# Kernel tuning notes

Hardware: AMD Instinct MI355X
Metric: run time of the kernel (lower is better)

Reference implementation:

```python
import jax, jax.numpy as jnp
import numpy as np

B, S, E, H = 16, 1024, 256, 8
DH = E // H


def layer_norm(x, g, b, eps=1e-5):
    m = jnp.mean(x, axis=-1, keepdims=True)
    v = jnp.mean(jnp.square(x - m), axis=-1, keepdims=True)
    return (x - m) * jax.lax.rsqrt(v + eps) * g + b


def setup_inputs() -> dict:
    key = jax.random.key(0)
    ks = jax.random.split(key, 8)
    w = 1.0 / np.sqrt(E)
    return {
        "Matrix": jax.random.normal(ks[0], (B, S, E), jnp.float32),
        "ln_g": jnp.ones((E,), jnp.float32),
        "ln_b": jnp.zeros((E,), jnp.float32),
        "Wq": jax.random.normal(ks[1], (E, E), jnp.float32) * w,
        "bq": jnp.zeros((E,), jnp.float32),
        "Wk": jax.random.normal(ks[2], (E, E), jnp.float32) * w,
        "bk": jnp.zeros((E,), jnp.float32),
        "Wv": jax.random.normal(ks[3], (E, E), jnp.float32) * w,
        "bv": jnp.zeros((E,), jnp.float32),
        "Wo": jax.random.normal(ks[4], (E, E), jnp.float32) * w,
        "bo": jnp.zeros((E,), jnp.float32),
        "rel_bias": jax.random.normal(ks[5], (S, S), jnp.float32) * 0.02,
        "gW": jax.random.normal(ks[6], (E, E), jnp.float32) * w,
        "gb": jnp.zeros((E,), jnp.float32),
        "mW": jax.random.normal(ks[7], (E, E), jnp.float32) * w,
        "mb": jnp.zeros((E,), jnp.float32),
    }


def relation_mha(x, Wq, bq, Wk, bk, Wv, bv, Wo, bo, rel_bias):
    # x: [B,S,E]; self-attention q=k=v=x with additive per-game-pair bias
    def heads(t):
        return t.reshape(B, S, H, DH).transpose(0, 2, 1, 3)  # [B,H,S,DH]
    q = heads(x @ Wq + bq)
    k = heads(x @ Wk + bk)
    v = heads(x @ Wv + bv)
    scores = jnp.einsum("bhqd,bhkd->bhqk", q, k) / np.sqrt(DH)
    scores = scores + rel_bias[None, None, :, :]  # relational bias over game pairs
    attn = jax.nn.softmax(scores, axis=-1)
    o = jnp.einsum("bhqk,bhkd->bhqd", attn, v)
    o = o.transpose(0, 2, 1, 3).reshape(B, S, E)
    return o @ Wo + bo


def reference(Matrix, ln_g, ln_b, Wq, bq, Wk, bk, Wv, bv, Wo, bo, rel_bias, gW, gb, mW, mb):
    ln = layer_norm(Matrix, ln_g, ln_b)
    rmha = relation_mha(ln, Wq, bq, Wk, bk, Wv, bv, Wo, bo, rel_bias)
    gate0 = jax.nn.sigmoid(Matrix @ gW + gb)
    gate1 = gate0 * rmha + Matrix
    mlp = jax.nn.sigmoid(gate1 @ mW + mb)
    final = gate1 * layer_norm(mlp, ln_g, ln_b) + gate1
    return final
```

## Files before the change

### kernel.cpp

```cpp
#include <hip/hip_runtime.h>
#include <hip/hip_bf16.h>


#define BB 16
#define SS 1024
#define EE 256
#define HH 8
#define DHD 32
#define MM (BB*SS)

typedef __attribute__((ext_vector_type(8))) short bf16x8;
typedef __attribute__((ext_vector_type(4))) float f32x4;
typedef __attribute__((ext_vector_type(4))) unsigned short u16x4;
typedef __attribute__((ext_vector_type(4))) _Float16 h16x4;
typedef __attribute__((ext_vector_type(8))) _Float16 h16x8;
typedef __attribute__((ext_vector_type(2))) _Float16 h16x2;

__device__ __forceinline__ float bf2f(unsigned short u){
  unsigned int x = ((unsigned int)u) << 16;
  return __builtin_bit_cast(float, x);
}
__device__ __forceinline__ unsigned short f2bf(float f){
  unsigned int x = __builtin_bit_cast(unsigned int, f);
  return (unsigned short)((x + 0x7FFFu + ((x >> 16) & 1u)) >> 16);
}

struct SP { const void* s[8]; };
__global__ __launch_bounds__(256) void conv_small(SP sp, unsigned short* __restrict__ dst,
    const unsigned int* __restrict__ lraw){
  bool isbf = (lraw[0] != 0x3F800000u);
  int a = blockIdx.x, t = threadIdx.x;
  const void* s = sp.s[a];
  dst[a*256 + t] = isbf ? ((const unsigned short*)s)[t] : f2bf(((const float*)s)[t]);
}

struct WSP { const void* s[6]; };
__global__ __launch_bounds__(256) void transp_w(WSP wp, unsigned short* __restrict__ dst,
    const unsigned int* __restrict__ lraw){
  __shared__ float T[64][65];
  bool isbf = (lraw[0] != 0x3F800000u);
  int w = blockIdx.z, k0 = blockIdx.x*64, n0 = blockIdx.y*64;
  int tx = threadIdx.x & 63, ty = threadIdx.x >> 6;
  const void* s = wp.s[w];
  #pragma unroll
  for (int r = ty; r < 64; r += 4)
    T[r][tx] = isbf ? bf2f(((const unsigned short*)s)[(k0+r)*EE + n0+tx])
                    : ((const float*)s)[(k0+r)*EE + n0+tx];
  __syncthreads();
  #pragma unroll
  for (int r = ty; r < 64; r += 4)
    dst[(size_t)w*EE*EE + (size_t)(n0+r)*EE + k0+tx] = f2bf(T[tx][r]);
}

__global__ __launch_bounds__(256) void rbh_prep(const void* __restrict__ src,
    unsigned short* __restrict__ dst, const unsigned int* __restrict__ lraw){
  bool isbf = (lraw[0] != 0x3F800000u);
  int idx = blockIdx.x*256 + threadIdx.x;
  int k4 = idx & (SS/4 - 1), q = idx >> 8;
  int k = k4*4;
  const float LOG2E = 1.4426950408889634f;
  float4 v;
  if (isbf){
    u16x4 u = ((const u16x4*)src)[idx];
    v.x = bf2f(u.x); v.y = bf2f(u.y); v.z = bf2f(u.z); v.w = bf2f(u.w);
  } else {
    v = ((const float4*)src)[idx];
  }
  u16x4 o;
  o.x = f2bf(v.x*LOG2E); o.y = f2bf(v.y*LOG2E);
  o.z = f2bf(v.z*LOG2E); o.w = f2bf(v.w*LOG2E);
  size_t base = ((size_t)(k >> 4)*SS + q)*16 + (k & 15);
  *(u16x4*)&dst[base] = o;
}

__global__ __launch_bounds__(256) void ln_x(const void* __restrict__ Mraw,
    const unsigned short* __restrict__ g, const unsigned short* __restrict__ b,
    unsigned short* __restrict__ Xc, unsigned short* __restrict__ LNout,
    const unsigned int* __restrict__ lraw){
  int wave = threadIdx.x >> 6, lane = threadIdx.x & 63;
  size_t row = (size_t)blockIdx.x*4 + wave;
  int col = lane*4;
  bool isbf = (lraw[0] != 0x3F800000u);
  float x0, x1, x2, x3;
  if (isbf){
    u16x4 xu = *(const u16x4*)((const unsigned short*)Mraw + row*EE + col);
    x0 = bf2f(xu.x); x1 = bf2f(xu.y); x2 = bf2f(xu.z); x3 = bf2f(xu.w);
  } else {
    float4 xv = *(const float4*)((const float*)Mraw + row*EE + col);
    x0 = xv.x; x1 = xv.y; x2 = xv.z; x3 = xv.w;
  }
  u16x4 xo; xo.x = f2bf(x0); xo.y = f2bf(x1); xo.z = f2bf(x2); xo.w = f2bf(x3);
  *(u16x4*)(Xc + row*EE + col) = xo;
  float s = (x0+x1)+(x2+x3);
  float s2 = (x0*x0+x1*x1)+(x2*x2+x3*x3);
  #pragma unroll
  for (int o = 32; o >= 1; o >>= 1){ s += __shfl_xor(s, o, 64); s2 += __shfl_xor(s2, o, 64); }
  float m = s*(1.0f/EE);
  float var = s2*(1.0f/EE) - m*m;
  float rstd = rsqrtf(var + 1e-5f);
  u16x4 gu = *(const u16x4*)(g + col), bu = *(const u16x4*)(b + col);
  u16x4 o;
  o.x = f2bf((x0-m)*rstd*bf2f(gu.x) + bf2f(bu.x));
  o.y = f2bf((x1-m)*rstd*bf2f(gu.y) + bf2f(bu.y));
  o.z = f2bf((x2-m)*rstd*bf2f(gu.z) + bf2f(bu.z));
  o.w = f2bf((x3-m)*rstd*bf2f(gu.w) + bf2f(bu.w));
  *(u16x4*)(LNout + row*EE + col) = o;
}

__global__ __launch_bounds__(256, 2) void qkv_gemm(const unsigned short* __restrict__ LN,
    const unsigned short* __restrict__ WqT, const unsigned short* __restrict__ WkT,
    const unsigned short* __restrict__ WvT, const unsigned short* __restrict__ bq,
    const unsigned short* __restrict__ bk, const unsigned short* __restrict__ bv,
    _Float16* __restrict__ Qh, _Float16* __restrict__ Kh, _Float16* __restrict__ Vf){
  int tid = threadIdx.x, wave = tid >> 6, lane = tid & 63, quad = lane >> 4, l16 = lane & 15;
  int mw = blockIdx.x*256 + wave*64;
  int n0 = blockIdx.y*32;
  const float QSCL = 0.2550348663f;
  f32x4 aq[4][2] = {}, ak[4][2] = {}, av[4][2] = {};
  const unsigned short* Ap = LN + (size_t)mw*EE;
  #pragma unroll
  for (int k0 = 0; k0 < EE; k0 += 32){
    bf16x8 a[4], b1[2], b2[2], b3[2];
    #pragma unroll
    for (int mf = 0; mf < 4; mf++)
      a[mf] = *(const bf16x8*)(Ap + (size_t)(mf*16 + l16)*EE + k0 + quad*8);
    #pragma unroll
    for (int nt = 0; nt < 2; nt++){
      b1[nt] = *(const bf16x8*)(WqT + (size_t)(n0 + nt*16 + l16)*EE + k0 + quad*8);
      b2[nt] = *(const bf16x8*)(WkT + (size_t)(n0 + nt*16 + l16)*EE + k0 + quad*8);
      b3[nt] = *(const bf16x8*)(WvT + (size_t)(n0 + nt*16 + l16)*EE + k0 + quad*8);
    }
    #pragma unroll
    for (int mf = 0; mf < 4; mf++)
      #pragma unroll
      for (int nt = 0; nt < 2; nt++){
        aq[mf][nt] = __builtin_amdgcn_mfma_f32_16x16x32_bf16(a[mf], b1[nt], aq[mf][nt], 0, 0, 0);
        ak[mf][nt] = __builtin_amdgcn_mfma_f32_16x16x32_bf16(a[mf], b2[nt], ak[mf][nt], 0, 0, 0);
        av[mf][nt] = __builtin_amdgcn_mfma_f32_16x16x32_bf16(a[mf], b3[nt], av[mf][nt], 0, 0, 0);
      }
  }
  int sblk = mw & 1023, bb = mw >> 10;
  #pragma unroll
  for (int nt = 0; nt < 2; nt++){
    int col = n0 + nt*16 + l16, hh = col >> 5, dd = col & 31;
    float bqv = bf2f(bq[col]), bkv = bf2f(bk[col]), bvv = bf2f(bv[col]);
    size_t bhh = (size_t)(bb*HH + hh);
    #pragma unroll
    for (int mf = 0; mf < 4; mf++){
      int s0 = sblk + mf*16 + quad*4;
      h16x4 vv;
      #pragma unroll
      for (int r = 0; r < 4; r++) vv[r] = (_Float16)(av[mf][nt][r] + bvv);
      *(h16x4*)(Vf + ((bhh*64 + (s0 >> 4))*DHD + dd)*16 + (s0 & 15)) = vv;
      #pragma unroll
      for (int r = 0; r < 4; r++){
        size_t o = (bhh*SS + s0 + r)*DHD + dd;
        Qh[o] = (_Float16)((aq[mf][nt][r] + bqv) * QSCL);
        Kh[o] = (_Float16)(ak[mf][nt][r] + bkv);
      }
    }
  }
}

__global__ __launch_bounds__(256) void attn(const _Float16* __restrict__ Qh,
    const _Float16* __restrict__ Kh, const _Float16* __restrict__ Vf,
    const unsigned short* __restrict__ RBh, unsigned short* __restrict__ O){
  int qt = blockIdx.x, h = blockIdx.y, b = blockIdx.z;
  int tid = threadIdx.x, wave = tid >> 6, lane = tid & 63, quad = lane >> 4, l16 = lane & 15;
  int q0 = qt*128 + wave*32;
  const size_t bh = (size_t)(b*HH + h);

  h16x8 qb[2];
  qb[0] = *(const h16x8*)(Qh + (bh*SS + q0 +      l16)*DHD + quad*8);
  qb[1] = *(const h16x8*)(Qh + (bh*SS + q0 + 16 + l16)*DHD + quad*8);

  const _Float16* kp = Kh + (bh*SS + l16)*DHD + quad*8;
  const _Float16* vp = Vf + (bh*64*DHD + l16)*16 + quad*4;
  const unsigned short* rp0 = RBh + ((size_t)0*SS + q0 + l16)*16 + quad*4;
  const unsigned short* rp1 = RBh + ((size_t)1*SS + q0 + l16)*16 + quad*4;
  const unsigned short* rp2 = RBh + ((size_t)2*SS + q0 + l16)*16 + quad*4;
  const unsigned short* rp3 = RBh + ((size_t)3*SS + q0 + l16)*16 + quad*4;

  f32x4 oacc[2][2] = {};
  f32x4 lac[2] = {};

  h16x8 kf[4];
  u16x4 rbu[4][2];
  kf[0] = *(const h16x8*)(kp +    0);
  kf[1] = *(const h16x8*)(kp +  512);
  kf[2] = *(const h16x8*)(kp + 1024);
  kf[3] = *(const h16x8*)(kp + 1536);
  rbu[0][0] = *(const u16x4*)(rp0); rbu[0][1] = *(const u16x4*)(rp0 + 256);
  rbu[1][0] = *(const u16x4*)(rp1); rbu[1][1] = *(const u16x4*)(rp1 + 256);
  rbu[2][0] = *(const u16x4*)(rp2); rbu[2][1] = *(const u16x4*)(rp2 + 256);
  rbu[3][0] = *(const u16x4*)(rp3); rbu[3][1] = *(const u16x4*)(rp3 + 256);
  kp += 2048; rp0 += 65536; rp1 += 65536; rp2 += 65536; rp3 += 65536;

  for (int kt = 0; kt < 16; kt++){
    h16x4 vf[4][2];
    #pragma unroll
    for (int c = 0; c < 4; c++){
      vf[c][0] = *(const h16x4*)(vp + (c*2    )*256);
      vf[c][1] = *(const h16x4*)(vp + (c*2 + 1)*256);
    }
    h16x8 kn[4];
    u16x4 rbn[4][2];
    if (kt < 15){
      kn[0] = *(const h16x8*)(kp +    0);
      kn[1] = *(const h16x8*)(kp +  512);
      kn[2] = *(const h16x8*)(kp + 1024);
      kn[3] = *(const h16x8*)(kp + 1536);
      rbn[0][0] = *(const u16x4*)(rp0); rbn[0][1] = *(const u16x4*)(rp0 + 256);
      rbn[1][0] = *(const u16x4*)(rp1); rbn[1][1] = *(const u16x4*)(rp1 + 256);
      rbn[2][0] = *(const u16x4*)(rp2); rbn[2][1] = *(const u16x4*)(rp2 + 256);
      rbn[3][0] = *(const u16x4*)(rp3); rbn[3][1] = *(const u16x4*)(rp3 + 256);
    }
    #pragma unroll
    for (int c = 0; c < 4; c++){
      #pragma unroll
      for (int qf = 0; qf < 2; qf++){
        f32x4 rb;
        rb[0] = bf2f(rbu[c][qf].x); rb[1] = bf2f(rbu[c][qf].y);
        rb[2] = bf2f(rbu[c][qf].z); rb[3] = bf2f(rbu[c][qf].w);
        f32x4 st = __builtin_amdgcn_mfma_f32_16x16x32_f16(kf[c], qb[qf], rb, 0, 0, 0);
        f32x4 p;
        p[0] = __builtin_amdgcn_exp2f(st[0]);
        p[1] = __builtin_amdgcn_exp2f(st[1]);
        p[2] = __builtin_amdgcn_exp2f(st[2]);
        p[3] = __builtin_amdgcn_exp2f(st[3]);
        lac[qf] += p;
        h16x2 lo = __builtin_bit_cast(h16x2, __builtin_amdgcn_cvt_pkrtz(p[0], p[1]));
        h16x2 hi = __builtin_bit_cast(h16x2, __builtin_amdgcn_cvt_pkrtz(p[2], p[3]));
        h16x4 pf; pf[0] = lo[0]; pf[1] = lo[1]; pf[2] = hi[0]; pf[3] = hi[1];
        oacc[qf][0] = __builtin_amdgcn_mfma_f32_16x16x16f16(pf, vf[c][0], oacc[qf][0], 0, 0, 0);
        oacc[qf][1] = __builtin_amdgcn_mfma_f32_16x16x16f16(pf, vf[c][1], oacc[qf][1], 0, 0, 0);
      }
    }
    #pragma unroll
    for (int c = 0; c < 4; c++){
      kf[c] = kn[c];
      rbu[c][0] = rbn[c][0]; rbu[c][1] = rbn[c][1];
    }
    kp += 2048; vp += 2048;
    rp0 += 65536; rp1 += 65536; rp2 += 65536; rp3 += 65536;
  }
  float lsum[2];
  #pragma unroll
  for (int qf = 0; qf < 2; qf++){
    float l = (lac[qf][0] + lac[qf][1]) + (lac[qf][2] + lac[qf][3]);
    l += __shfl_xor(l, 16, 64);
    l += __shfl_xor(l, 32, 64);
    lsum[qf] = l;
  }
  #pragma unroll
  for (int qf = 0; qf < 2; qf++)
    #pragma unroll
    for (int r = 0; r < 4; r++){
      float linv = 1.0f / __shfl(lsum[qf], quad*4 + r, 64);
      int q = q0 + qf*16 + quad*4 + r;
      #pragma unroll
      for (int dt = 0; dt < 2; dt++)
        O[((size_t)(b*SS + q))*EE + h*DHD + dt*16 + l16] = f2bf(oacc[qf][dt][r] * linv);
    }
}

__global__ __launch_bounds__(256, 2) void og_gemm(const unsigned short* __restrict__ AO,
    const unsigned short* __restrict__ Xc, const unsigned short* __restrict__ WoT,
    const unsigned short* __restrict__ gWT, const unsigned short* __restrict__ bo,
    const unsigned short* __restrict__ gb, unsigned short* __restrict__ G1b){
  int tid = threadIdx.x, wave = tid >> 6, lane = tid & 63, quad = lane >> 4, l16 = lane & 15;
  int mw = blockIdx.x*256 + wave*64;
  int n0 = blockIdx.y*32;
  f32x4 ro[4][2] = {}, rg[4][2] = {};
  #pragma unroll
  for (int k0 = 0; k0 < EE; k0 += 32){
    bf16x8 a1[4], a2[4], b1[2], b2[2];
    #pragma unroll
    for (int mf = 0; mf < 4; mf++){
      a1[mf] = *(const bf16x8*)(AO + (size_t)(mw + mf*16 + l16)*EE + k0 + quad*8);
      a2[mf] = *(const bf16x8*)(Xc + (size_t)(mw + mf*16 + l16)*EE + k0 + quad*8);
    }
    #pragma unroll
    for (int nt = 0; nt < 2; nt++){
      b1[nt] = *(const bf16x8*)(WoT + (size_t)(n0 + nt*16 + l16)*EE + k0 + quad*8);
      b2[nt] = *(const bf16x8*)(gWT + (size_t)(n0 + nt*16 + l16)*EE + k0 + quad*8);
    }
    #pragma unroll
    for (int mf = 0; mf < 4; mf++)
      #pragma unroll
      for (int nt = 0; nt < 2; nt++){
        ro[mf][nt] = __builtin_amdgcn_mfma_f32_16x16x32_bf16(a1[mf], b1[nt], ro[mf][nt], 0, 0, 0);
        rg[mf][nt] = __builtin_amdgcn_mfma_f32_16x16x32_bf16(a2[mf], b2[nt], rg[mf][nt], 0, 0, 0);
      }
  }
  #pragma unroll
  for (int nt = 0; nt < 2; nt++){
    int col = n0 + nt*16 + l16;
    float bov = bf2f(bo[col]), gbv = bf2f(gb[col]);
    #pragma unroll
    for (int mf = 0; mf < 4; mf++)
      #pragma unroll
      for (int r = 0; r < 4; r++){
        size_t row = (size_t)(mw + mf*16 + quad*4 + r);
        float rm  = ro[mf][nt][r] + bov;
        float g0p = rg[mf][nt][r] + gbv;
        float g0  = 1.0f / (1.0f + __expf(-g0p));
        float x   = bf2f(Xc[row*EE + col]);
        G1b[row*EE + col] = f2bf(g0*rm + x);
      }
  }
}

__global__ __launch_bounds__(256, 4) void mlp_final(const unsigned short* __restrict__ G1,
    const unsigned short* __restrict__ Wt, const unsigned short* __restrict__ bias,
    const unsigned short* __restrict__ g, const unsigned short* __restrict__ b,
    void* __restrict__ out, const unsigned int* __restrict__ lraw){
  __shared__ float red[4][16][2];
  int tid = threadIdx.x, wave = tid >> 6, lane = tid & 63, quad = lane >> 4, l16 = lane & 15;
  int m0 = blockIdx.x*16;
  int n0 = wave*64;
  f32x4 acc[4] = {};
  const unsigned short* Ap = G1 + (size_t)(m0 + l16)*EE + quad*8;
  #pragma unroll
  for (int k0 = 0; k0 < EE; k0 += 32){
    bf16x8 a = *(const bf16x8*)(Ap + k0);
    #pragma unroll
    for (int nt = 0; nt < 4; nt++){
      bf16x8 bb = *(const bf16x8*)(Wt + (size_t)(n0 + nt*16 + l16)*EE + k0 + quad*8);
      acc[nt] = __builtin_amdgcn_mfma_f32_16x16x32_bf16(a, bb, acc[nt], 0, 0, 0);
    }
  }
  #pragma unroll
  for (int nt = 0; nt < 4; nt++){
    float bv = bf2f(bias[n0 + nt*16 + l16]);
    #pragma unroll
    for (int r = 0; r < 4; r++)
      acc[nt][r] = 1.0f / (1.0f + __expf(-(acc[nt][r] + bv)));
  }
  #pragma unroll
  for (int r = 0; r < 4; r++){
    float s  = (acc[0][r] + acc[1][r]) + (acc[2][r] + acc[3][r]);
    float sq = (acc[0][r]*acc[0][r] + acc[1][r]*acc[1][r])
             + (acc[2][r]*acc[2][r] + acc[3][r]*acc[3][r]);
    #pragma unroll
    for (int o = 8; o >= 1; o >>= 1){ s += __shfl_xor(s, o, 64); sq += __shfl_xor(sq, o, 64); }
    if (l16 == 0){ red[wave][quad*4 + r][0] = s; red[wave][quad*4 + r][1] = sq; }
  }
  __syncthreads();
  bool isbf = (lraw[0] != 0x3F800000u);
  #pragma unroll
  for (int r = 0; r < 4; r++){
    int rowl = quad*4 + r;
    float s  = (red[0][rowl][0] + red[1][rowl][0]) + (red[2][rowl][0] + red[3][rowl][0]);
    float sq = (red[0][rowl][1] + red[1][rowl][1]) + (red[2][rowl][1] + red[3][rowl][1]);
    float m = s*(1.0f/EE);
    float var = sq*(1.0f/EE) - m*m;
    float rstd = rsqrtf(var + 1e-5f);
    size_t row = (size_t)(m0 + rowl);
    #pragma unroll
    for (int nt = 0; nt < 4; nt++){
      int col = n0 + nt*16 + l16;
      float ln = (acc[nt][r] - m)*rstd*bf2f(g[col]) + bf2f(b[col]);
      float g1 = bf2f(G1[row*EE + col]);
      float y = g1*ln + g1;
      if (isbf) ((unsigned short*)out)[row*EE + col] = f2bf(y);
      else      ((float*)out)[row*EE + col] = y;
    }
  }
}

extern "C" void kernel_launch(void* const* d_in, const int* in_sizes, int n_in,
                              void* d_out, int out_size, void* d_ws, size_t ws_size,
                              hipStream_t stream) {
  (void)in_sizes; (void)n_in; (void)out_size; (void)ws_size;
  const unsigned int* lraw = (const unsigned int*)d_in[1];

  char* ws = (char*)d_ws;
  size_t off = 0;
  auto alloc = [&](size_t bytes)->char*{
    char* p = ws + off; off += (bytes + 255) & ~(size_t)255; return p;
  };
  unsigned short* Xc  = (unsigned short*)alloc((size_t)MM*EE*2);
  unsigned short* RBh = (unsigned short*)alloc((size_t)SS*SS*2);
  unsigned short* SM  = (unsigned short*)alloc(8*256*2);
  unsigned short* Wt  = (unsigned short*)alloc((size_t)6*EE*EE*2);
  unsigned short* LNb = (unsigned short*)alloc((size_t)MM*EE*2);
  _Float16*       Qh  = (_Float16*)alloc((size_t)MM*EE*2);
  _Float16*       Kh  = (_Float16*)alloc((size_t)MM*EE*2);
  _Float16*       Vf  = (_Float16*)alloc((size_t)MM*EE*2);
  unsigned short* AOut= (unsigned short*)alloc((size_t)MM*EE*2);
  unsigned short* G1b = (unsigned short*)alloc((size_t)MM*EE*2);

  dim3 b256(256);
  SP sp = {{ d_in[1], d_in[2], d_in[4], d_in[6], d_in[8], d_in[10], d_in[13], d_in[15] }};
  conv_small<<<dim3(8), b256, 0, stream>>>(sp, SM, lraw);
  WSP wp = {{ d_in[3], d_in[5], d_in[7], d_in[9], d_in[12], d_in[14] }};
  transp_w<<<dim3(4, 4, 6), b256, 0, stream>>>(wp, Wt, lraw);
  rbh_prep<<<dim3(SS*SS/4/256), b256, 0, stream>>>(d_in[11], RBh, lraw);

  ln_x<<<dim3(MM/4), b256, 0, stream>>>(d_in[0], SM + 0*256, SM + 1*256, Xc, LNb, lraw);

  qkv_gemm<<<dim3(64, 8), b256, 0, stream>>>(LNb, Wt + 0*EE*EE, Wt + 1*EE*EE, Wt + 2*EE*EE,
                                             SM + 2*256, SM + 3*256, SM + 4*256, Qh, Kh, Vf);

  attn<<<dim3(8, 8, 16), b256, 0, stream>>>(Qh, Kh, Vf, RBh, AOut);

  og_gemm<<<dim3(64, 8), b256, 0, stream>>>(AOut, Xc, Wt + 3*EE*EE, Wt + 4*EE*EE,
                                            SM + 5*256, SM + 6*256, G1b);

  mlp_final<<<dim3(MM/16), b256, 0, stream>>>(G1b, Wt + 5*EE*EE, SM + 7*256,
                                              SM + 0*256, SM + 1*256, d_out, lraw);
}
```

Measured before the change: 238.3 us.

## Shrink attention per-wave query tile to 16 rows and reorder grid by head

```diff
diff --git a/kernel.cpp b/kernel.cpp
--- a/kernel.cpp
+++ b/kernel.cpp
@@ -162,106 +162,83 @@
   }
 }
 
-__global__ __launch_bounds__(256) void attn(const _Float16* __restrict__ Qh,
+__global__ __launch_bounds__(256, 6) void attn(const _Float16* __restrict__ Qh,
     const _Float16* __restrict__ Kh, const _Float16* __restrict__ Vf,
     const unsigned short* __restrict__ RBh, unsigned short* __restrict__ O){
-  int qt = blockIdx.x, h = blockIdx.y, b = blockIdx.z;
+  int h = blockIdx.x, qt = blockIdx.y, b = blockIdx.z;
   int tid = threadIdx.x, wave = tid >> 6, lane = tid & 63, quad = lane >> 4, l16 = lane & 15;
-  int q0 = qt*128 + wave*32;
+  int q0 = qt*64 + wave*16;
   const size_t bh = (size_t)(b*HH + h);
 
-  h16x8 qb[2];
-  qb[0] = *(const h16x8*)(Qh + (bh*SS + q0 +      l16)*DHD + quad*8);
-  qb[1] = *(const h16x8*)(Qh + (bh*SS + q0 + 16 + l16)*DHD + quad*8);
+  h16x8 qb = *(const h16x8*)(Qh + (bh*SS + q0 + l16)*DHD + quad*8);
 
   const _Float16* kp = Kh + (bh*SS + l16)*DHD + quad*8;
   const _Float16* vp = Vf + (bh*64*DHD + l16)*16 + quad*4;
-  const unsigned short* rp0 = RBh + ((size_t)0*SS + q0 + l16)*16 + quad*4;
-  const unsigned short* rp1 = RBh + ((size_t)1*SS + q0 + l16)*16 + quad*4;
-  const unsigned short* rp2 = RBh + ((size_t)2*SS + q0 + l16)*16 + quad*4;
-  const unsigned short* rp3 = RBh + ((size_t)3*SS + q0 + l16)*16 + quad*4;
-
-  f32x4 oacc[2][2] = {};
-  f32x4 lac[2] = {};
+  const unsigned short* rp = RBh + ((size_t)q0 + l16)*16 + quad*4;
+
+  f32x4 oacc[2] = {};
+  f32x4 lac = {};
 
   h16x8 kf[4];
-  u16x4 rbu[4][2];
+  u16x4 rbu[4];
   kf[0] = *(const h16x8*)(kp +    0);
   kf[1] = *(const h16x8*)(kp +  512);
   kf[2] = *(const h16x8*)(kp + 1024);
   kf[3] = *(const h16x8*)(kp + 1536);
-  rbu[0][0] = *(const u16x4*)(rp0); rbu[0][1] = *(const u16x4*)(rp0 + 256);
-  rbu[1][0] = *(const u16x4*)(rp1); rbu[1][1] = *(const u16x4*)(rp1 + 256);
-  rbu[2][0] = *(const u16x4*)(rp2); rbu[2][1] = *(const u16x4*)(rp2 + 256);
-  rbu[3][0] = *(const u16x4*)(rp3); rbu[3][1] = *(const u16x4*)(rp3 + 256);
-  kp += 2048; rp0 += 65536; rp1 += 65536; rp2 += 65536; rp3 += 65536;
+  rbu[0] = *(const u16x4*)(rp +     0);
+  rbu[1] = *(const u16x4*)(rp + 16384);
+  rbu[2] = *(const u16x4*)(rp + 32768);
+  rbu[3] = *(const u16x4*)(rp + 49152);
+  kp += 2048; rp += 65536;
 
   for (int kt = 0; kt < 16; kt++){
-    h16x4 vf[4][2];
-    #pragma unroll
-    for (int c = 0; c < 4; c++){
-      vf[c][0] = *(const h16x4*)(vp + (c*2    )*256);
-      vf[c][1] = *(const h16x4*)(vp + (c*2 + 1)*256);
-    }
     h16x8 kn[4];
-    u16x4 rbn[4][2];
+    u16x4 rbn[4];
     if (kt < 15){
       kn[0] = *(const h16x8*)(kp +    0);
       kn[1] = *(const h16x8*)(kp +  512);
       kn[2] = *(const h16x8*)(kp + 1024);
       kn[3] = *(const h16x8*)(kp + 1536);
-      rbn[0][0] = *(const u16x4*)(rp0); rbn[0][1] = *(const u16x4*)(rp0 + 256);
-      rbn[1][0] = *(const u16x4*)(rp1); rbn[1][1] = *(const u16x4*)(rp1 + 256);
-      rbn[2][0] = *(const u16x4*)(rp2); rbn[2][1] = *(const u16x4*)(rp2 + 256);
-      rbn[3][0] = *(const u16x4*)(rp3); rbn[3][1] = *(const u16x4*)(rp3 + 256);
+      rbn[0] = *(const u16x4*)(rp +     0);
+      rbn[1] = *(const u16x4*)(rp + 16384);
+      rbn[2] = *(const u16x4*)(rp + 32768);
+      rbn[3] = *(const u16x4*)(rp + 49152);
     }
     #pragma unroll
     for (int c = 0; c < 4; c++){
-      #pragma unroll
-      for (int qf = 0; qf < 2; qf++){
-        f32x4 rb;
-        rb[0] = bf2f(rbu[c][qf].x); rb[1] = bf2f(rbu[c][qf].y);
-        rb[2] = bf2f(rbu[c][qf].z); rb[3] = bf2f(rbu[c][qf].w);
-        f32x4 st = __builtin_amdgcn_mfma_f32_16x16x32_f16(kf[c], qb[qf], rb, 0, 0, 0);
-        f32x4 p;
-        p[0] = __builtin_amdgcn_exp2f(st[0]);
-        p[1] = __builtin_amdgcn_exp2f(st[1]);
-        p[2] = __builtin_amdgcn_exp2f(st[2]);
-        p[3] = __builtin_amdgcn_exp2f(st[3]);
-        lac[qf] += p;
-        h16x2 lo = __builtin_bit_cast(h16x2, __builtin_amdgcn_cvt_pkrtz(p[0], p[1]));
-        h16x2 hi = __builtin_bit_cast(h16x2, __builtin_amdgcn_cvt_pkrtz(p[2], p[3]));
-        h16x4 pf; pf[0] = lo[0]; pf[1] = lo[1]; pf[2] = hi[0]; pf[3] = hi[1];
-        oacc[qf][0] = __builtin_amdgcn_mfma_f32_16x16x16f16(pf, vf[c][0], oacc[qf][0], 0, 0, 0);
-        oacc[qf][1] = __builtin_amdgcn_mfma_f32_16x16x16f16(pf, vf[c][1], oacc[qf][1], 0, 0, 0);
-      }
-    }
-    #pragma unroll
-    for (int c = 0; c < 4; c++){
-      kf[c] = kn[c];
-      rbu[c][0] = rbn[c][0]; rbu[c][1] = rbn[c][1];
-    }
-    kp += 2048; vp += 2048;
-    rp0 += 65536; rp1 += 65536; rp2 += 65536; rp3 += 65536;
-  }
-  float lsum[2];
-  #pragma unroll
-  for (int qf = 0; qf < 2; qf++){
-    float l = (lac[qf][0] + lac[qf][1]) + (lac[qf][2] + lac[qf][3]);
-    l += __shfl_xor(l, 16, 64);
-    l += __shfl_xor(l, 32, 64);
-    lsum[qf] = l;
-  }
-  #pragma unroll
-  for (int qf = 0; qf < 2; qf++)
-    #pragma unroll
-    for (int r = 0; r < 4; r++){
-      float linv = 1.0f / __shfl(lsum[qf], quad*4 + r, 64);
-      int q = q0 + qf*16 + quad*4 + r;
-      #pragma unroll
-      for (int dt = 0; dt < 2; dt++)
-        O[((size_t)(b*SS + q))*EE + h*DHD + dt*16 + l16] = f2bf(oacc[qf][dt][r] * linv);
-    }
+      h16x4 vf0 = *(const h16x4*)(vp + (c*2    )*256);
+      h16x4 vf1 = *(const h16x4*)(vp + (c*2 + 1)*256);
+      f32x4 rb;
+      rb[0] = bf2f(rbu[c].x); rb[1] = bf2f(rbu[c].y);
+      rb[2] = bf2f(rbu[c].z); rb[3] = bf2f(rbu[c].w);
+      f32x4 st = __builtin_amdgcn_mfma_f32_16x16x32_f16(kf[c], qb, rb, 0, 0, 0);
+      f32x4 p;
+      p[0] = __builtin_amdgcn_exp2f(st[0]);
+      p[1] = __builtin_amdgcn_exp2f(st[1]);
+      p[2] = __builtin_amdgcn_exp2f(st[2]);
+      p[3] = __builtin_amdgcn_exp2f(st[3]);
+      lac += p;
+      h16x2 lo = __builtin_bit_cast(h16x2, __builtin_amdgcn_cvt_pkrtz(p[0], p[1]));
+      h16x2 hi = __builtin_bit_cast(h16x2, __builtin_amdgcn_cvt_pkrtz(p[2], p[3]));
+      h16x4 pf; pf[0] = lo[0]; pf[1] = lo[1]; pf[2] = hi[0]; pf[3] = hi[1];
+      oacc[0] = __builtin_amdgcn_mfma_f32_16x16x16f16(pf, vf0, oacc[0], 0, 0, 0);
+      oacc[1] = __builtin_amdgcn_mfma_f32_16x16x16f16(pf, vf1, oacc[1], 0, 0, 0);
+    }
+    #pragma unroll
+    for (int c = 0; c < 4; c++){ kf[c] = kn[c]; rbu[c] = rbn[c]; }
+    kp += 2048; vp += 2048; rp += 65536;
+  }
+  float l = (lac[0] + lac[1]) + (lac[2] + lac[3]);
+  l += __shfl_xor(l, 16, 64);
+  l += __shfl_xor(l, 32, 64);
+  #pragma unroll
+  for (int r = 0; r < 4; r++){
+    float linv = 1.0f / __shfl(l, quad*4 + r, 64);
+    int q = q0 + quad*4 + r;
+    #pragma unroll
+    for (int dt = 0; dt < 2; dt++)
+      O[((size_t)(b*SS + q))*EE + h*DHD + dt*16 + l16] = f2bf(oacc[dt][r] * linv);
+  }
 }
 
 __global__ __launch_bounds__(256, 2) void og_gemm(const unsigned short* __restrict__ AO,
@@ -403,7 +380,7 @@
   qkv_gemm<<<dim3(64, 8), b256, 0, stream>>>(LNb, Wt + 0*EE*EE, Wt + 1*EE*EE, Wt + 2*EE*EE,
                                              SM + 2*256, SM + 3*256, SM + 4*256, Qh, Kh, Vf);
 
-  attn<<<dim3(8, 8, 16), b256, 0, stream>>>(Qh, Kh, Vf, RBh, AOut);
+  attn<<<dim3(8, 16, 16), b256, 0, stream>>>(Qh, Kh, Vf, RBh, AOut);
 
   og_gemm<<<dim3(64, 8), b256, 0, stream>>>(AOut, Xc, Wt + 3*EE*EE, Wt + 4*EE*EE,
                                             SM + 5*256, SM + 6*256, G1b);
```

Result: slower. 273.8 us (+14.9%).

## Retile rel-bias layout, prefetch V, and compute softmax row sums via MFMA

Applied to the files above, without the earlier changes.

```diff
diff --git a/kernel.cpp b/kernel.cpp
--- a/kernel.cpp
+++ b/kernel.cpp
@@ -69,7 +69,8 @@
   u16x4 o;
   o.x = f2bf(v.x*LOG2E); o.y = f2bf(v.y*LOG2E);
   o.z = f2bf(v.z*LOG2E); o.w = f2bf(v.w*LOG2E);
-  size_t base = ((size_t)(k >> 4)*SS + q)*16 + (k & 15);
+  size_t base = (size_t)(q >> 5)*32768 + (size_t)(k >> 4)*512
+              + (size_t)((q >> 4) & 1)*256 + (size_t)(q & 15)*16 + (k & 15);
   *(u16x4*)&dst[base] = o;
 }
 
@@ -162,10 +163,10 @@
   }
 }
 
-__global__ __launch_bounds__(256) void attn(const _Float16* __restrict__ Qh,
+__global__ __launch_bounds__(256, 4) void attn(const _Float16* __restrict__ Qh,
     const _Float16* __restrict__ Kh, const _Float16* __restrict__ Vf,
     const unsigned short* __restrict__ RBh, unsigned short* __restrict__ O){
-  int qt = blockIdx.x, h = blockIdx.y, b = blockIdx.z;
+  int h = blockIdx.x, qt = blockIdx.y, b = blockIdx.z;
   int tid = threadIdx.x, wave = tid >> 6, lane = tid & 63, quad = lane >> 4, l16 = lane & 15;
   int q0 = qt*128 + wave*32;
   const size_t bh = (size_t)(b*HH + h);
@@ -176,44 +177,47 @@
 
   const _Float16* kp = Kh + (bh*SS + l16)*DHD + quad*8;
   const _Float16* vp = Vf + (bh*64*DHD + l16)*16 + quad*4;
-  const unsigned short* rp0 = RBh + ((size_t)0*SS + q0 + l16)*16 + quad*4;
-  const unsigned short* rp1 = RBh + ((size_t)1*SS + q0 + l16)*16 + quad*4;
-  const unsigned short* rp2 = RBh + ((size_t)2*SS + q0 + l16)*16 + quad*4;
-  const unsigned short* rp3 = RBh + ((size_t)3*SS + q0 + l16)*16 + quad*4;
+  const unsigned short* rp = RBh + (size_t)(q0 >> 5)*32768 + (size_t)l16*16 + quad*4;
 
   f32x4 oacc[2][2] = {};
-  f32x4 lac[2] = {};
+  f32x4 lacc[2] = {};
+  h16x4 ones;
+  ones[0] = (_Float16)1.0f; ones[1] = (_Float16)1.0f;
+  ones[2] = (_Float16)1.0f; ones[3] = (_Float16)1.0f;
 
   h16x8 kf[4];
   u16x4 rbu[4][2];
+  h16x4 vf[4][2];
   kf[0] = *(const h16x8*)(kp +    0);
   kf[1] = *(const h16x8*)(kp +  512);
   kf[2] = *(const h16x8*)(kp + 1024);
   kf[3] = *(const h16x8*)(kp + 1536);
-  rbu[0][0] = *(const u16x4*)(rp0); rbu[0][1] = *(const u16x4*)(rp0 + 256);
-  rbu[1][0] = *(const u16x4*)(rp1); rbu[1][1] = *(const u16x4*)(rp1 + 256);
-  rbu[2][0] = *(const u16x4*)(rp2); rbu[2][1] = *(const u16x4*)(rp2 + 256);
-  rbu[3][0] = *(const u16x4*)(rp3); rbu[3][1] = *(const u16x4*)(rp3 + 256);
-  kp += 2048; rp0 += 65536; rp1 += 65536; rp2 += 65536; rp3 += 65536;
-
+  #pragma unroll
+  for (int c = 0; c < 4; c++){
+    rbu[c][0] = *(const u16x4*)(rp + c*512);
+    rbu[c][1] = *(const u16x4*)(rp + c*512 + 256);
+    vf[c][0]  = *(const h16x4*)(vp + (c*2    )*256);
+    vf[c][1]  = *(const h16x4*)(vp + (c*2 + 1)*256);
+  }
+  kp += 2048; vp += 2048; rp += 2048;
+
+  #pragma unroll 2
   for (int kt = 0; kt < 16; kt++){
-    h16x4 vf[4][2];
-    #pragma unroll
-    for (int c = 0; c < 4; c++){
-      vf[c][0] = *(const h16x4*)(vp + (c*2    )*256);
-      vf[c][1] = *(const h16x4*)(vp + (c*2 + 1)*256);
-    }
     h16x8 kn[4];
     u16x4 rbn[4][2];
+    h16x4 vn[4][2];
     if (kt < 15){
       kn[0] = *(const h16x8*)(kp +    0);
       kn[1] = *(const h16x8*)(kp +  512);
       kn[2] = *(const h16x8*)(kp + 1024);
       kn[3] = *(const h16x8*)(kp + 1536);
-      rbn[0][0] = *(const u16x4*)(rp0); rbn[0][1] = *(const u16x4*)(rp0 + 256);
-      rbn[1][0] = *(const u16x4*)(rp1); rbn[1][1] = *(const u16x4*)(rp1 + 256);
-      rbn[2][0] = *(const u16x4*)(rp2); rbn[2][1] = *(const u16x4*)(rp2 + 256);
-      rbn[3][0] = *(const u16x4*)(rp3); rbn[3][1] = *(const u16x4*)(rp3 + 256);
+      #pragma unroll
+      for (int c = 0; c < 4; c++){
+        rbn[c][0] = *(const u16x4*)(rp + c*512);
+        rbn[c][1] = *(const u16x4*)(rp + c*512 + 256);
+        vn[c][0]  = *(const h16x4*)(vp + (c*2    )*256);
+        vn[c][1]  = *(const h16x4*)(vp + (c*2 + 1)*256);
+      }
     }
     #pragma unroll
     for (int c = 0; c < 4; c++){
@@ -228,35 +232,27 @@
         p[1] = __builtin_amdgcn_exp2f(st[1]);
         p[2] = __builtin_amdgcn_exp2f(st[2]);
         p[3] = __builtin_amdgcn_exp2f(st[3]);
-        lac[qf] += p;
         h16x2 lo = __builtin_bit_cast(h16x2, __builtin_amdgcn_cvt_pkrtz(p[0], p[1]));
         h16x2 hi = __builtin_bit_cast(h16x2, __builtin_amdgcn_cvt_pkrtz(p[2], p[3]));
         h16x4 pf; pf[0] = lo[0]; pf[1] = lo[1]; pf[2] = hi[0]; pf[3] = hi[1];
         oacc[qf][0] = __builtin_amdgcn_mfma_f32_16x16x16f16(pf, vf[c][0], oacc[qf][0], 0, 0, 0);
         oacc[qf][1] = __builtin_amdgcn_mfma_f32_16x16x16f16(pf, vf[c][1], oacc[qf][1], 0, 0, 0);
+        lacc[qf]    = __builtin_amdgcn_mfma_f32_16x16x16f16(pf, ones,     lacc[qf],    0, 0, 0);
       }
     }
     #pragma unroll
     for (int c = 0; c < 4; c++){
       kf[c] = kn[c];
       rbu[c][0] = rbn[c][0]; rbu[c][1] = rbn[c][1];
-    }
-    kp += 2048; vp += 2048;
-    rp0 += 65536; rp1 += 65536; rp2 += 65536; rp3 += 65536;
-  }
-  float lsum[2];
-  #pragma unroll
-  for (int qf = 0; qf < 2; qf++){
-    float l = (lac[qf][0] + lac[qf][1]) + (lac[qf][2] + lac[qf][3]);
-    l += __shfl_xor(l, 16, 64);
-    l += __shfl_xor(l, 32, 64);
-    lsum[qf] = l;
+      vf[c][0] = vn[c][0];   vf[c][1] = vn[c][1];
+    }
+    kp += 2048; vp += 2048; rp += 2048;
   }
   #pragma unroll
   for (int qf = 0; qf < 2; qf++)
     #pragma unroll
     for (int r = 0; r < 4; r++){
-      float linv = 1.0f / __shfl(lsum[qf], quad*4 + r, 64);
+      float linv = 1.0f / lacc[qf][r];
       int q = q0 + qf*16 + quad*4 + r;
       #pragma unroll
       for (int dt = 0; dt < 2; dt++)
```

After: 258.5 us. +8.5%, slower.

## Stage K/V tiles through LDS with async global_load_lds double buffering

Applied to the files above, without the earlier changes.

```diff
diff --git a/kernel.cpp b/kernel.cpp
--- a/kernel.cpp
+++ b/kernel.cpp
@@ -23,6 +23,12 @@
 __device__ __forceinline__ unsigned short f2bf(float f){
   unsigned int x = __builtin_bit_cast(unsigned int, f);
   return (unsigned short)((x + 0x7FFFu + ((x >> 16) & 1u)) >> 16);
+}
+
+__device__ __forceinline__ void gl16(const _Float16* g, _Float16* l){
+  __builtin_amdgcn_global_load_lds(
+      (const __attribute__((address_space(1))) unsigned int*)g,
+      (__attribute__((address_space(3))) unsigned int*)l, 16, 0, 0);
 }
 
 struct SP { const void* s[8]; };
@@ -145,27 +151,30 @@
     int col = n0 + nt*16 + l16, hh = col >> 5, dd = col & 31;
     float bqv = bf2f(bq[col]), bkv = bf2f(bk[col]), bvv = bf2f(bv[col]);
     size_t bhh = (size_t)(bb*HH + hh);
+    size_t tbase = bhh*32768 + (size_t)(sblk >> 6)*2048;
     #pragma unroll
     for (int mf = 0; mf < 4; mf++){
       int s0 = sblk + mf*16 + quad*4;
       h16x4 vv;
       #pragma unroll
       for (int r = 0; r < 4; r++) vv[r] = (_Float16)(av[mf][nt][r] + bvv);
-      *(h16x4*)(Vf + ((bhh*64 + (s0 >> 4))*DHD + dd)*16 + (s0 & 15)) = vv;
+      size_t vb = tbase + (size_t)(mf*2 + (dd >> 4))*256 + (size_t)(quad*16 + (dd & 15))*4;
+      *(h16x4*)(Vf + vb) = vv;
+      size_t kb = tbase + (size_t)mf*512 + (size_t)(dd >> 3)*128 + quad*32 + (dd & 7);
       #pragma unroll
       for (int r = 0; r < 4; r++){
-        size_t o = (bhh*SS + s0 + r)*DHD + dd;
-        Qh[o] = (_Float16)((aq[mf][nt][r] + bqv) * QSCL);
-        Kh[o] = (_Float16)(ak[mf][nt][r] + bkv);
+        Qh[(bhh*SS + s0 + r)*DHD + dd] = (_Float16)((aq[mf][nt][r] + bqv) * QSCL);
+        Kh[kb + r*8] = (_Float16)(ak[mf][nt][r] + bkv);
       }
     }
   }
 }
 
-__global__ __launch_bounds__(256) void attn(const _Float16* __restrict__ Qh,
+__global__ __launch_bounds__(256, 4) void attn(const _Float16* __restrict__ Qh,
     const _Float16* __restrict__ Kh, const _Float16* __restrict__ Vf,
     const unsigned short* __restrict__ RBh, unsigned short* __restrict__ O){
-  int qt = blockIdx.x, h = blockIdx.y, b = blockIdx.z;
+  __shared__ _Float16 lds[2][4096];
+  int h = blockIdx.x, qt = blockIdx.y, b = blockIdx.z;
   int tid = threadIdx.x, wave = tid >> 6, lane = tid & 63, quad = lane >> 4, l16 = lane & 15;
   int q0 = qt*128 + wave*32;
   const size_t bh = (size_t)(b*HH + h);
@@ -174,8 +183,8 @@
   qb[0] = *(const h16x8*)(Qh + (bh*SS + q0 +      l16)*DHD + quad*8);
   qb[1] = *(const h16x8*)(Qh + (bh*SS + q0 + 16 + l16)*DHD + quad*8);
 
-  const _Float16* kp = Kh + (bh*SS + l16)*DHD + quad*8;
-  const _Float16* vp = Vf + (bh*64*DHD + l16)*16 + quad*4;
+  const _Float16* kg = Kh + bh*32768 + tid*8;
+  const _Float16* vg = Vf + bh*32768 + tid*8;
   const unsigned short* rp0 = RBh + ((size_t)0*SS + q0 + l16)*16 + quad*4;
   const unsigned short* rp1 = RBh + ((size_t)1*SS + q0 + l16)*16 + quad*4;
   const unsigned short* rp2 = RBh + ((size_t)2*SS + q0 + l16)*16 + quad*4;
@@ -184,37 +193,37 @@
   f32x4 oacc[2][2] = {};
   f32x4 lac[2] = {};
 
-  h16x8 kf[4];
+  gl16(kg, &lds[0][tid*8]);
+  gl16(vg, &lds[0][2048 + tid*8]);
   u16x4 rbu[4][2];
-  kf[0] = *(const h16x8*)(kp +    0);
-  kf[1] = *(const h16x8*)(kp +  512);
-  kf[2] = *(const h16x8*)(kp + 1024);
-  kf[3] = *(const h16x8*)(kp + 1536);
   rbu[0][0] = *(const u16x4*)(rp0); rbu[0][1] = *(const u16x4*)(rp0 + 256);
   rbu[1][0] = *(const u16x4*)(rp1); rbu[1][1] = *(const u16x4*)(rp1 + 256);
   rbu[2][0] = *(const u16x4*)(rp2); rbu[2][1] = *(const u16x4*)(rp2 + 256);
   rbu[3][0] = *(const u16x4*)(rp3); rbu[3][1] = *(const u16x4*)(rp3 + 256);
-  kp += 2048; rp0 += 65536; rp1 += 65536; rp2 += 65536; rp3 += 65536;
+  rp0 += 65536; rp1 += 65536; rp2 += 65536; rp3 += 65536;
+  __syncthreads();
 
   for (int kt = 0; kt < 16; kt++){
-    h16x4 vf[4][2];
-    #pragma unroll
-    for (int c = 0; c < 4; c++){
-      vf[c][0] = *(const h16x4*)(vp + (c*2    )*256);
-      vf[c][1] = *(const h16x4*)(vp + (c*2 + 1)*256);
-    }
-    h16x8 kn[4];
+    int buf = kt & 1;
     u16x4 rbn[4][2];
     if (kt < 15){
-      kn[0] = *(const h16x8*)(kp +    0);
-      kn[1] = *(const h16x8*)(kp +  512);
-      kn[2] = *(const h16x8*)(kp + 1024);
-      kn[3] = *(const h16x8*)(kp + 1536);
+      gl16(kg + (kt+1)*2048, &lds[buf^1][tid*8]);
+      gl16(vg + (kt+1)*2048, &lds[buf^1][2048 + tid*8]);
       rbn[0][0] = *(const u16x4*)(rp0); rbn[0][1] = *(const u16x4*)(rp0 + 256);
       rbn[1][0] = *(const u16x4*)(rp1); rbn[1][1] = *(const u16x4*)(rp1 + 256);
       rbn[2][0] = *(const u16x4*)(rp2); rbn[2][1] = *(const u16x4*)(rp2 + 256);
       rbn[3][0] = *(const u16x4*)(rp3); rbn[3][1] = *(const u16x4*)(rp3 + 256);
     }
+    const _Float16* Kb = &lds[buf][0];
+    const _Float16* Vb = &lds[buf][2048];
+    h16x8 kfr[4];
+    h16x4 vfr[4][2];
+    #pragma unroll
+    for (int c = 0; c < 4; c++){
+      kfr[c]    = *(const h16x8*)(Kb + c*512 + lane*8);
+      vfr[c][0] = *(const h16x4*)(Vb + (c*2    )*256 + lane*4);
+      vfr[c][1] = *(const h16x4*)(Vb + (c*2 + 1)*256 + lane*4);
+    }
     #pragma unroll
     for (int c = 0; c < 4; c++){
       #pragma unroll
@@ -222,7 +231,7 @@
         f32x4 rb;
         rb[0] = bf2f(rbu[c][qf].x); rb[1] = bf2f(rbu[c][qf].y);
         rb[2] = bf2f(rbu[c][qf].z); rb[3] = bf2f(rbu[c][qf].w);
-        f32x4 st = __builtin_amdgcn_mfma_f32_16x16x32_f16(kf[c], qb[qf], rb, 0, 0, 0);
+        f32x4 st = __builtin_amdgcn_mfma_f32_16x16x32_f16(kfr[c], qb[qf], rb, 0, 0, 0);
         f32x4 p;
         p[0] = __builtin_amdgcn_exp2f(st[0]);
         p[1] = __builtin_amdgcn_exp2f(st[1]);
@@ -232,17 +241,16 @@
         h16x2 lo = __builtin_bit_cast(h16x2, __builtin_amdgcn_cvt_pkrtz(p[0], p[1]));
         h16x2 hi = __builtin_bit_cast(h16x2, __builtin_amdgcn_cvt_pkrtz(p[2], p[3]));
         h16x4 pf; pf[0] = lo[0]; pf[1] = lo[1]; pf[2] = hi[0]; pf[3] = hi[1];
-        oacc[qf][0] = __builtin_amdgcn_mfma_f32_16x16x16f16(pf, vf[c][0], oacc[qf][0], 0, 0, 0);
-        oacc[qf][1] = __builtin_amdgcn_mfma_f32_16x16x16f16(pf, vf[c][1], oacc[qf][1], 0, 0, 0);
+        oacc[qf][0] = __builtin_amdgcn_mfma_f32_16x16x16f16(pf, vfr[c][0], oacc[qf][0], 0, 0, 0);
+        oacc[qf][1] = __builtin_amdgcn_mfma_f32_16x16x16f16(pf, vfr[c][1], oacc[qf][1], 0, 0, 0);
       }
     }
     #pragma unroll
     for (int c = 0; c < 4; c++){
-      kf[c] = kn[c];
       rbu[c][0] = rbn[c][0]; rbu[c][1] = rbn[c][1];
     }
-    kp += 2048; vp += 2048;
     rp0 += 65536; rp1 += 65536; rp2 += 65536; rp3 += 65536;
+    __syncthreads();
   }
   float lsum[2];
   #pragma unroll
```

Result: faster. 219.8 us (-7.7%).
